# Performance work log

Measured on AMD Instinct MI355X. Metric: run time of the kernel, lower is better.

Reference implementation:

```python
import jax, jax.numpy as jnp
import numpy as np

N = 50000      # nodes
E = 1600000    # edges (avg degree 32)
IN, HID, OUT = 32, 32, 10
K = 2          # kernel_size (dim=1, degree=1 open B-spline -> basis (1-u, u))


def setup_inputs() -> dict:
    key = jax.random.key(0)
    ks = jax.random.split(key, 10)
    x = jax.random.normal(ks[0], (N, IN), dtype=jnp.float32)
    edge_index = jax.random.randint(ks[1], (2, E), 0, N, dtype=jnp.int64)
    edge_attr = jax.random.uniform(ks[2], (E, 1), dtype=jnp.float32)  # pseudo-coords in [0,1)
    s1 = 1.0 / np.sqrt(IN * K)
    s2 = 1.0 / np.sqrt(HID * K)
    W1 = jax.random.uniform(ks[3], (K, IN, HID), minval=-s1, maxval=s1, dtype=jnp.float32)
    root1 = jax.random.uniform(ks[4], (IN, HID), minval=-s1, maxval=s1, dtype=jnp.float32)
    b1 = jnp.zeros((HID,), jnp.float32)
    W2 = jax.random.uniform(ks[5], (K, HID, OUT), minval=-s2, maxval=s2, dtype=jnp.float32)
    root2 = jax.random.uniform(ks[6], (HID, OUT), minval=-s2, maxval=s2, dtype=jnp.float32)
    b2 = jnp.zeros((OUT,), jnp.float32)
    return {"x": x, "edge_index": edge_index, "edge_attr": edge_attr,
            "W1": W1, "root1": root1, "b1": b1,
            "W2": W2, "root2": root2, "b2": b2}


def spline_conv(x, edge_index, edge_attr, W, W_root, b):
    # SplineConv, dim=1, kernel_size=2, degree=1, aggr='mean', root_weight, bias.
    # Basis for pseudo u in [0,1): B_0(u) = 1-u, B_1(u) = u.
    src, dst = edge_index[0], edge_index[1]
    u = edge_attr[:, 0]                      # [E]
    h0 = x @ W[0]                            # [N, out] node-level transform, then gather
    h1 = x @ W[1]
    msg = (1.0 - u)[:, None] * h0[src] + u[:, None] * h1[src]   # [E, out]
    n = x.shape[0]
    agg = jax.ops.segment_sum(msg, dst, num_segments=n)
    deg = jax.ops.segment_sum(jnp.ones((src.shape[0],), x.dtype), dst, num_segments=n)
    mean = agg / jnp.maximum(deg, 1.0)[:, None]
    return mean + x @ W_root + b


def reference(x, edge_index, edge_attr, W1, root1, b1, W2, root2, b2):
    # Dropout is identity in eval mode.
    h = jax.nn.relu(spline_conv(x, edge_index, edge_attr, W1, root1, b1))
    h = spline_conv(h, edge_index, edge_attr, W2, root2, b2)
    return jax.nn.log_softmax(h, axis=1)
```

## Files before the change

kernel.cpp:

```cpp
#include <hip/hip_runtime.h>
#include <math.h>

#define GSHIFT 6
#define GSIZE  64
#define NBSZ   1024
#define EPB    4096
#define CAP    3072

#define UDEC1 0.00390625f
#define UDEC2 0.001953125f

__device__ __forceinline__ unsigned bf16rn(float f) {
    unsigned u = __float_as_uint(f);
    return (u + 0x7FFFu + ((u >> 16) & 1u)) >> 16;
}
__device__ __forceinline__ float bfl(unsigned v) { return __uint_as_float(v << 16); }
__device__ __forceinline__ float bfh(unsigned v) { return __uint_as_float(v & 0xFFFF0000u); }

__global__ __launch_bounds__(256) void k_prep(const float* __restrict__ x,
                                              unsigned* __restrict__ x_pk,
                                              int* __restrict__ bcount,
                                              int n, int NB) {
    int t = blockIdx.x * 256 + threadIdx.x;
    if (t < NB) bcount[t] = 0;
    if (t >= n) return;
    const float4* xp = (const float4*)(x + (size_t)t * 32);
    #pragma unroll
    for (int k = 0; k < 4; k++) {
        float4 a = xp[2 * k], c = xp[2 * k + 1];
        uint4 pk;
        pk.x = bf16rn(a.x) | (bf16rn(a.y) << 16);
        pk.y = bf16rn(a.z) | (bf16rn(a.w) << 16);
        pk.z = bf16rn(c.x) | (bf16rn(c.y) << 16);
        pk.w = bf16rn(c.z) | (bf16rn(c.w) << 16);
        *(uint4*)(x_pk + (size_t)t * 16 + k * 4) = pk;
    }
}

__global__ __launch_bounds__(1024) void k_part(const int* __restrict__ src,
                                               const int* __restrict__ dst,
                                               const float* __restrict__ attr,
                                               int* __restrict__ bcount,
                                               unsigned* __restrict__ su,
                                               int E_, int NB) {
    __shared__ int lh[NBSZ];
    __shared__ int lst[NBSZ];
    __shared__ int lcur[NBSZ];
    __shared__ int gbase[NBSZ];
    __shared__ int wsum[16];
    __shared__ __align__(16) unsigned srt[EPB];
    __shared__ unsigned short lbk[EPB];
    int tid = threadIdx.x, lane = tid & 63, w = tid >> 6;
    lh[tid] = 0;
    __syncthreads();
    int base = blockIdx.x * EPB;
    int d[4];
    unsigned rec[4];
    #pragma unroll
    for (int k = 0; k < 4; k++) {
        int e = base + k * 1024 + tid;
        bool val = e < E_;
        int dd = val ? dst[e] : 0;
        int s  = val ? src[e] : 0;
        float a = val ? attr[e] : 0.f;
        d[k] = val ? (dd >> GSHIFT) : -1;
        unsigned uq = (unsigned)(a * 256.0f);
        rec[k] = (unsigned)(s & 0xFFFF) | ((unsigned)(dd & (GSIZE - 1)) << 16) | (uq << 24);
        if (d[k] >= 0) atomicAdd(&lh[d[k]], 1);
    }
    __syncthreads();
    int v = lh[tid];
    int incl = v;
    #pragma unroll
    for (int o = 1; o < 64; o <<= 1) {
        int t2 = __shfl_up(incl, o);
        if (lane >= o) incl += t2;
    }
    if (lane == 63) wsum[w] = incl;
    __syncthreads();
    int woff = 0;
    for (int k = 0; k < w; k++) woff += wsum[k];
    int excl = woff + incl - v;
    lst[tid] = excl;
    lcur[tid] = excl;
    if (tid < NB) gbase[tid] = atomicAdd(&bcount[tid], v);
    __syncthreads();
    #pragma unroll
    for (int k = 0; k < 4; k++) {
        if (d[k] >= 0) {
            int pos = atomicAdd(&lcur[d[k]], 1);
            srt[pos] = rec[k];
            lbk[pos] = (unsigned short)d[k];
        }
    }
    __syncthreads();
    int total = E_ - base; if (total > EPB) total = EPB;
    for (int p = tid; p < total; p += 1024) {
        int b = lbk[p];
        su[(size_t)b * CAP + gbase[b] + (p - lst[b])] = srt[p];
    }
}

__global__ __launch_bounds__(512) void k_fused(const int* __restrict__ bcount,
                                               const unsigned* __restrict__ su,
                                               unsigned* __restrict__ su2,
                                               int* __restrict__ rowptr,
                                               int* __restrict__ deg,
                                               const unsigned* __restrict__ x_pk,
                                               const float* __restrict__ x,
                                               const float* __restrict__ W1,
                                               const float* __restrict__ root1,
                                               const float* __restrict__ b1,
                                               const float* __restrict__ W2,
                                               const float* __restrict__ root2,
                                               unsigned* __restrict__ gg,
                                               float* __restrict__ hr, int n) {
    __shared__ __align__(16) float sW0[1024], sDl[1024], sRt[1024];
    __shared__ float sA0[320], sD2[320], sR2[320], sB1[32];
    __shared__ __align__(16) unsigned sorted[CAP];
    __shared__ __align__(16) float accum[GSIZE * 64];
    __shared__ __align__(16) float xl[GSIZE * 32];
    __shared__ __align__(16) float hl[GSIZE * 32];
    __shared__ int hist[GSIZE], cur[GSIZE], sstart[GSIZE], sdeg[GSIZE];
    __shared__ int stot;

    int b = blockIdx.x, tid = threadIdx.x;
    size_t basee = (size_t)b * CAP;
    int cnt = bcount[b];
    int node0 = b << GSHIFT;

    if (tid < GSIZE) hist[tid] = 0;
    for (int i = tid; i < 1024; i += 512) {
        float w0 = W1[i];
        sW0[i] = w0; sDl[i] = W1[1024 + i] - w0; sRt[i] = root1[i];
    }
    for (int i = tid; i < 320; i += 512) {
        float a0 = W2[i];
        sA0[i] = a0; sD2[i] = W2[320 + i] - a0; sR2[i] = root2[i];
    }
    if (tid < 32) sB1[tid] = b1[tid];
    {
        size_t xbase = (size_t)node0 * 32;
        size_t xlim = (size_t)n * 32;
        for (int i = tid; i < GSIZE * 32; i += 512)
            xl[i] = (xbase + i < xlim) ? x[xbase + i] : 0.f;
    }
    __syncthreads();

    for (int e = tid; e < cnt; e += 512)
        atomicAdd(&hist[(su[basee + e] >> 16) & 63], 1);
    __syncthreads();

    if (tid < 64) {
        int v = hist[tid];
        int pv = (v + 3) & ~3;
        int incl = pv;
        #pragma unroll
        for (int o = 1; o < 64; o <<= 1) {
            int t2 = __shfl_up(incl, o);
            if (tid >= o) incl += t2;
        }
        int excl = incl - pv;
        cur[tid] = excl; sstart[tid] = excl; sdeg[tid] = v;
        int node = node0 + tid;
        if (node < n) { rowptr[node] = (int)basee + excl; deg[node] = v; }
        if (tid == 63) stot = excl + pv;
        for (int p = excl + v; p < excl + pv; p++) sorted[p] = 0;
    }
    __syncthreads();

    for (int e = tid; e < cnt; e += 512) {
        unsigned r = su[basee + e];
        int pos = atomicAdd(&cur[(r >> 16) & 63], 1);
        sorted[pos] = r;
    }
    __syncthreads();

    {
        int tot4 = stot >> 2;
        uint4* dp = (uint4*)(su2 + basee);
        for (int p = tid; p < tot4; p += 512)
            dp[p] = *(const uint4*)(sorted + p * 4);
    }
    {
        int nl = tid >> 3, q = tid & 3, half = (tid >> 2) & 1;
        int st = sstart[nl], dgi = sdeg[nl];
        int endl = st + dgi;
        int q4 = (dgi + 3) >> 2;
        int hq = q4 >> 1, rem = q4 & 1;
        int myq = hq + (half < rem ? 1 : 0);
        int e0 = st + (half * hq + min(half, rem)) * 4;
        float a0[8] = {0,0,0,0,0,0,0,0}, a1[8] = {0,0,0,0,0,0,0,0};
        for (int i = 0; i < myq; i++) {
            int e = e0 + i * 4;
            uint4 rq = *(const uint4*)(sorted + e);
            unsigned rr[4] = {rq.x, rq.y, rq.z, rq.w};
            #pragma unroll
            for (int k = 0; k < 4; k++) {
                bool v = (e + k) < endl;
                unsigned r = rr[k];
                uint4 g = *(const uint4*)(x_pk + (size_t)(r & 0xFFFFu) * 16 + q * 4);
                float wv = v ? 1.f : 0.f;
                float u = v ? fmaf((float)(r >> 24), UDEC1, UDEC2) : 0.f;
                unsigned gw[4] = {g.x, g.y, g.z, g.w};
                #pragma unroll
                for (int m2 = 0; m2 < 4; m2++) {
                    float fl = bfl(gw[m2]), fh = bfh(gw[m2]);
                    a0[2*m2]   = fmaf(wv, fl, a0[2*m2]);
                    a0[2*m2+1] = fmaf(wv, fh, a0[2*m2+1]);
                    a1[2*m2]   = fmaf(u, fl, a1[2*m2]);
                    a1[2*m2+1] = fmaf(u, fh, a1[2*m2+1]);
                }
            }
        }
        #pragma unroll
        for (int k = 0; k < 8; k++) {
            a0[k] += __shfl_xor(a0[k], 4);
            a1[k] += __shfl_xor(a1[k], 4);
        }
        if (half == 0) {
            #pragma unroll
            for (int k = 0; k < 8; k++) {
                accum[nl * 64 + q * 8 + k]      = a0[k];
                accum[nl * 64 + 32 + q * 8 + k] = a1[k];
            }
        }
    }
    __syncthreads();

    {
        int nl = tid >> 3, j = tid & 7;
        float invd = 1.0f / fmaxf((float)sdeg[nl], 1.0f);
        float4 hv = *(const float4*)(sB1 + 0);
        hv.x = sB1[4*j]; hv.y = sB1[4*j+1]; hv.z = sB1[4*j+2]; hv.w = sB1[4*j+3];
        for (int i = 0; i < 32; i++) {
            float s0 = accum[nl * 64 + i] * invd;
            float s1 = accum[nl * 64 + 32 + i] * invd;
            float xi = xl[nl * 32 + i];
            float4 w0 = *(const float4*)(sW0 + i * 32 + 4 * j);
            float4 dl = *(const float4*)(sDl + i * 32 + 4 * j);
            float4 rt = *(const float4*)(sRt + i * 32 + 4 * j);
            hv.x = fmaf(s0, w0.x, fmaf(s1, dl.x, fmaf(xi, rt.x, hv.x)));
            hv.y = fmaf(s0, w0.y, fmaf(s1, dl.y, fmaf(xi, rt.y, hv.y)));
            hv.z = fmaf(s0, w0.z, fmaf(s1, dl.z, fmaf(xi, rt.z, hv.z)));
            hv.w = fmaf(s0, w0.w, fmaf(s1, dl.w, fmaf(xi, rt.w, hv.w)));
        }
        hv.x = fmaxf(hv.x, 0.f); hv.y = fmaxf(hv.y, 0.f);
        hv.z = fmaxf(hv.z, 0.f); hv.w = fmaxf(hv.w, 0.f);
        *(float4*)(hl + nl * 32 + 4 * j) = hv;
    }
    __syncthreads();

    {
        int nl = tid >> 3, j = tid & 7;
        int node = node0 + nl;
        if (node < n) {
            #pragma unroll
            for (int ci = 0; ci < 2; ci++) {
                int c = j + ci * 8;
                if (c < 10) {
                    float g0 = 0.f, gd = 0.f, gr = 0.f;
                    for (int i = 0; i < 32; i++) {
                        float hi = hl[nl * 32 + i];
                        g0 = fmaf(hi, sA0[i * 10 + c], g0);
                        gd = fmaf(hi, sD2[i * 10 + c], gd);
                        gr = fmaf(hi, sR2[i * 10 + c], gr);
                    }
                    gg[(size_t)node * 16 + c] = bf16rn(g0) | (bf16rn(gd) << 16);
                    hr[(size_t)node * 10 + c] = gr;
                } else {
                    gg[(size_t)node * 16 + c] = 0;
                }
            }
        }
    }
}

__global__ __launch_bounds__(256) void k_agg2(const int* __restrict__ rowptr,
                                              const int* __restrict__ deg,
                                              const unsigned* __restrict__ su2,
                                              const unsigned* __restrict__ gg,
                                              const float* __restrict__ hr,
                                              const float* __restrict__ b2,
                                              float* __restrict__ out, int n) {
    int lane = threadIdx.x & 63;
    int node = (blockIdx.x * 4 + (threadIdx.x >> 6)) * 4 + (lane >> 4);
    int qt = (lane >> 2) & 3;
    int q  = lane & 3;
    if (node >= n) return;
    int start = rowptr[node], dgi = deg[node], end = start + dgi;
    int q4 = (dgi + 3) >> 2;
    int qb = q4 >> 2, rem = q4 & 3;
    int myq = qb + (qt < rem ? 1 : 0);
    int e0 = start + (qt * qb + min(qt, rem)) * 4;
    float acc[4] = {0, 0, 0, 0};
    for (int i = 0; i < myq; i++) {
        int e = e0 + i * 4;
        uint4 rq = *(const uint4*)(su2 + e);
        unsigned rr[4] = {rq.x, rq.y, rq.z, rq.w};
        #pragma unroll
        for (int k = 0; k < 4; k++) {
            bool v = (e + k) < end;
            unsigned r = rr[k];
            uint4 g = *(const uint4*)(gg + (size_t)(r & 0xFFFFu) * 16 + q * 4);
            float wv = v ? 1.f : 0.f;
            float u = v ? fmaf((float)(r >> 24), UDEC1, UDEC2) : 0.f;
            acc[0] = fmaf(wv, bfl(g.x), fmaf(u, bfh(g.x), acc[0]));
            acc[1] = fmaf(wv, bfl(g.y), fmaf(u, bfh(g.y), acc[1]));
            acc[2] = fmaf(wv, bfl(g.z), fmaf(u, bfh(g.z), acc[2]));
            acc[3] = fmaf(wv, bfl(g.w), fmaf(u, bfh(g.w), acc[3]));
        }
    }
    #pragma unroll
    for (int k = 0; k < 4; k++) {
        acc[k] += __shfl_xor(acc[k], 4);
        acc[k] += __shfl_xor(acc[k], 8);
    }
    float invd = 1.0f / fmaxf((float)dgi, 1.0f);
    int c0 = q * 4;
    float lg[4];
    float m = -INFINITY;
    #pragma unroll
    for (int k = 0; k < 4; k++) {
        int c = c0 + k;
        if (c < 10) {
            lg[k] = fmaf(acc[k], invd, hr[(size_t)node * 10 + c] + b2[c]);
            m = fmaxf(m, lg[k]);
        } else lg[k] = -INFINITY;
    }
    m = fmaxf(m, __shfl_xor(m, 1));
    m = fmaxf(m, __shfl_xor(m, 2));
    float ex = 0.f;
    #pragma unroll
    for (int k = 0; k < 4; k++)
        if (c0 + k < 10) ex += __expf(lg[k] - m);
    ex += __shfl_xor(ex, 1);
    ex += __shfl_xor(ex, 2);
    float lse = m + __logf(ex);
    if (qt == 0 && c0 < 10) {
        *(float2*)(out + (size_t)node * 10 + c0) =
            make_float2(lg[0] - lse, lg[1] - lse);
        if (c0 + 2 < 10)
            *(float2*)(out + (size_t)node * 10 + c0 + 2) =
                make_float2(lg[2] - lse, lg[3] - lse);
    }
}

extern "C" void kernel_launch(void* const* d_in, const int* in_sizes, int n_in,
                              void* d_out, int out_size, void* d_ws, size_t ws_size,
                              hipStream_t stream) {
    const float* x     = (const float*)d_in[0];
    const int*   ei    = (const int*)d_in[1];
    const float* attr  = (const float*)d_in[2];
    const float* W1    = (const float*)d_in[3];
    const float* root1 = (const float*)d_in[4];
    const float* b1    = (const float*)d_in[5];
    const float* W2    = (const float*)d_in[6];
    const float* root2 = (const float*)d_in[7];
    const float* b2    = (const float*)d_in[8];
    float* out = (float*)d_out;

    int N_ = in_sizes[0] / 32;
    int E_ = in_sizes[1] / 2;
    const int* src = ei;
    const int* dst = ei + E_;
    int NB = (N_ + GSIZE - 1) >> GSHIFT;
    int NP = (E_ + EPB - 1) / EPB;

    char* ws = (char*)d_ws;
    size_t off = 0;
    auto alloc = [&](size_t bytes) -> void* {
        void* p = ws + off;
        off += (bytes + 255) & ~(size_t)255;
        return p;
    };
    int*      bcount = (int*)     alloc((size_t)NB * 4);
    unsigned* su     = (unsigned*)alloc(((size_t)NB * CAP + 64) * 4);
    unsigned* su2    = (unsigned*)alloc(((size_t)NB * CAP + 64) * 4);
    int*      rowptr = (int*)     alloc((size_t)N_ * 4);
    int*      deg    = (int*)     alloc((size_t)N_ * 4);
    unsigned* x_pk   = (unsigned*)alloc((size_t)N_ * 16 * 4);
    unsigned* gg     = (unsigned*)alloc((size_t)N_ * 16 * 4);
    float*    hr     = (float*)   alloc((size_t)N_ * 10 * 4);

    int prep_blocks = (N_ > NB ? N_ : NB);
    k_prep <<<(prep_blocks + 255) / 256, 256, 0, stream>>>(x, x_pk, bcount, N_, NB);
    k_part <<<NP, 1024, 0, stream>>>(src, dst, attr, bcount, su, E_, NB);
    k_fused<<<NB, 512, 0, stream>>>(bcount, su, su2, rowptr, deg, x_pk, x,
                                    W1, root1, b1, W2, root2, gg, hr, N_);
    k_agg2 <<<(N_ + 15) / 16, 256, 0, stream>>>(rowptr, deg, su2, gg, hr, b2, out, N_);
}
```

Baseline: 82.33 us.

## Double k_fused block size to 1024 threads with 16 threads per node

The fused layer-1 kernel now launches 1024 threads per block instead of 512. In the gather, each node's edge quads are split over four thread groups instead of two, with an extra xor-shuffle reduction. The dense layer-1 and layer-2 transforms are remapped to 16 threads per node. This adds memory-level parallelism to the latency-bound gather and removes the two-pass loop in the layer-2 output. The cost is fewer resident blocks per CU, plus extra shuffles and per-thread work that becomes too small.

New measurement: 87.53 us. +6.3%, slower.

```diff
diff --git a/kernel.cpp b/kernel.cpp
--- a/kernel.cpp
+++ b/kernel.cpp
@@ -101,20 +101,20 @@
     }
 }
 
-__global__ __launch_bounds__(512) void k_fused(const int* __restrict__ bcount,
-                                               const unsigned* __restrict__ su,
-                                               unsigned* __restrict__ su2,
-                                               int* __restrict__ rowptr,
-                                               int* __restrict__ deg,
-                                               const unsigned* __restrict__ x_pk,
-                                               const float* __restrict__ x,
-                                               const float* __restrict__ W1,
-                                               const float* __restrict__ root1,
-                                               const float* __restrict__ b1,
-                                               const float* __restrict__ W2,
-                                               const float* __restrict__ root2,
-                                               unsigned* __restrict__ gg,
-                                               float* __restrict__ hr, int n) {
+__global__ __launch_bounds__(1024) void k_fused(const int* __restrict__ bcount,
+                                                const unsigned* __restrict__ su,
+                                                unsigned* __restrict__ su2,
+                                                int* __restrict__ rowptr,
+                                                int* __restrict__ deg,
+                                                const unsigned* __restrict__ x_pk,
+                                                const float* __restrict__ x,
+                                                const float* __restrict__ W1,
+                                                const float* __restrict__ root1,
+                                                const float* __restrict__ b1,
+                                                const float* __restrict__ W2,
+                                                const float* __restrict__ root2,
+                                                unsigned* __restrict__ gg,
+                                                float* __restrict__ hr, int n) {
     __shared__ __align__(16) float sW0[1024], sDl[1024], sRt[1024];
     __shared__ float sA0[320], sD2[320], sR2[320], sB1[32];
     __shared__ __align__(16) unsigned sorted[CAP];
@@ -130,24 +130,24 @@
     int node0 = b << GSHIFT;
 
     if (tid < GSIZE) hist[tid] = 0;
-    for (int i = tid; i < 1024; i += 512) {
-        float w0 = W1[i];
-        sW0[i] = w0; sDl[i] = W1[1024 + i] - w0; sRt[i] = root1[i];
-    }
-    for (int i = tid; i < 320; i += 512) {
-        float a0 = W2[i];
-        sA0[i] = a0; sD2[i] = W2[320 + i] - a0; sR2[i] = root2[i];
+    if (tid < 1024) {
+        float w0 = W1[tid];
+        sW0[tid] = w0; sDl[tid] = W1[1024 + tid] - w0; sRt[tid] = root1[tid];
+    }
+    if (tid < 320) {
+        float a0 = W2[tid];
+        sA0[tid] = a0; sD2[tid] = W2[320 + tid] - a0; sR2[tid] = root2[tid];
     }
     if (tid < 32) sB1[tid] = b1[tid];
     {
         size_t xbase = (size_t)node0 * 32;
         size_t xlim = (size_t)n * 32;
-        for (int i = tid; i < GSIZE * 32; i += 512)
+        for (int i = tid; i < GSIZE * 32; i += 1024)
             xl[i] = (xbase + i < xlim) ? x[xbase + i] : 0.f;
     }
     __syncthreads();
 
-    for (int e = tid; e < cnt; e += 512)
+    for (int e = tid; e < cnt; e += 1024)
         atomicAdd(&hist[(su[basee + e] >> 16) & 63], 1);
     __syncthreads();
 
@@ -169,7 +169,7 @@
     }
     __syncthreads();
 
-    for (int e = tid; e < cnt; e += 512) {
+    for (int e = tid; e < cnt; e += 1024) {
         unsigned r = su[basee + e];
         int pos = atomicAdd(&cur[(r >> 16) & 63], 1);
         sorted[pos] = r;
@@ -179,17 +179,17 @@
     {
         int tot4 = stot >> 2;
         uint4* dp = (uint4*)(su2 + basee);
-        for (int p = tid; p < tot4; p += 512)
+        for (int p = tid; p < tot4; p += 1024)
             dp[p] = *(const uint4*)(sorted + p * 4);
     }
     {
-        int nl = tid >> 3, q = tid & 3, half = (tid >> 2) & 1;
+        int nl = tid >> 4, qt = (tid >> 2) & 3, q = tid & 3;
         int st = sstart[nl], dgi = sdeg[nl];
         int endl = st + dgi;
         int q4 = (dgi + 3) >> 2;
-        int hq = q4 >> 1, rem = q4 & 1;
-        int myq = hq + (half < rem ? 1 : 0);
-        int e0 = st + (half * hq + min(half, rem)) * 4;
+        int qb = q4 >> 2, rem = q4 & 3;
+        int myq = qb + (qt < rem ? 1 : 0);
+        int e0 = st + (qt * qb + min(qt, rem)) * 4;
         float a0[8] = {0,0,0,0,0,0,0,0}, a1[8] = {0,0,0,0,0,0,0,0};
         for (int i = 0; i < myq; i++) {
             int e = e0 + i * 4;
@@ -217,8 +217,10 @@
         for (int k = 0; k < 8; k++) {
             a0[k] += __shfl_xor(a0[k], 4);
             a1[k] += __shfl_xor(a1[k], 4);
-        }
-        if (half == 0) {
+            a0[k] += __shfl_xor(a0[k], 8);
+            a1[k] += __shfl_xor(a1[k], 8);
+        }
+        if (qt == 0) {
             #pragma unroll
             for (int k = 0; k < 8; k++) {
                 accum[nl * 64 + q * 8 + k]      = a0[k];
@@ -229,48 +231,40 @@
     __syncthreads();
 
     {
-        int nl = tid >> 3, j = tid & 7;
+        int nl = tid >> 4, j = tid & 15;
         float invd = 1.0f / fmaxf((float)sdeg[nl], 1.0f);
-        float4 hv = *(const float4*)(sB1 + 0);
-        hv.x = sB1[4*j]; hv.y = sB1[4*j+1]; hv.z = sB1[4*j+2]; hv.w = sB1[4*j+3];
+        float hx = sB1[2*j], hy = sB1[2*j+1];
         for (int i = 0; i < 32; i++) {
             float s0 = accum[nl * 64 + i] * invd;
             float s1 = accum[nl * 64 + 32 + i] * invd;
             float xi = xl[nl * 32 + i];
-            float4 w0 = *(const float4*)(sW0 + i * 32 + 4 * j);
-            float4 dl = *(const float4*)(sDl + i * 32 + 4 * j);
-            float4 rt = *(const float4*)(sRt + i * 32 + 4 * j);
-            hv.x = fmaf(s0, w0.x, fmaf(s1, dl.x, fmaf(xi, rt.x, hv.x)));
-            hv.y = fmaf(s0, w0.y, fmaf(s1, dl.y, fmaf(xi, rt.y, hv.y)));
-            hv.z = fmaf(s0, w0.z, fmaf(s1, dl.z, fmaf(xi, rt.z, hv.z)));
-            hv.w = fmaf(s0, w0.w, fmaf(s1, dl.w, fmaf(xi, rt.w, hv.w)));
-        }
-        hv.x = fmaxf(hv.x, 0.f); hv.y = fmaxf(hv.y, 0.f);
-        hv.z = fmaxf(hv.z, 0.f); hv.w = fmaxf(hv.w, 0.f);
-        *(float4*)(hl + nl * 32 + 4 * j) = hv;
-    }
-    __syncthreads();
-
-    {
-        int nl = tid >> 3, j = tid & 7;
+            float2 w0 = *(const float2*)(sW0 + i * 32 + 2 * j);
+            float2 dl = *(const float2*)(sDl + i * 32 + 2 * j);
+            float2 rt = *(const float2*)(sRt + i * 32 + 2 * j);
+            hx = fmaf(s0, w0.x, fmaf(s1, dl.x, fmaf(xi, rt.x, hx)));
+            hy = fmaf(s0, w0.y, fmaf(s1, dl.y, fmaf(xi, rt.y, hy)));
+        }
+        hx = fmaxf(hx, 0.f); hy = fmaxf(hy, 0.f);
+        *(float2*)(hl + nl * 32 + 2 * j) = make_float2(hx, hy);
+    }
+    __syncthreads();
+
+    {
+        int nl = tid >> 4, c = tid & 15;
         int node = node0 + nl;
         if (node < n) {
-            #pragma unroll
-            for (int ci = 0; ci < 2; ci++) {
-                int c = j + ci * 8;
-                if (c < 10) {
-                    float g0 = 0.f, gd = 0.f, gr = 0.f;
-                    for (int i = 0; i < 32; i++) {
-                        float hi = hl[nl * 32 + i];
-                        g0 = fmaf(hi, sA0[i * 10 + c], g0);
-                        gd = fmaf(hi, sD2[i * 10 + c], gd);
-                        gr = fmaf(hi, sR2[i * 10 + c], gr);
-                    }
-                    gg[(size_t)node * 16 + c] = bf16rn(g0) | (bf16rn(gd) << 16);
-                    hr[(size_t)node * 10 + c] = gr;
-                } else {
-                    gg[(size_t)node * 16 + c] = 0;
+            if (c < 10) {
+                float g0 = 0.f, gd = 0.f, gr = 0.f;
+                for (int i = 0; i < 32; i++) {
+                    float hi = hl[nl * 32 + i];
+                    g0 = fmaf(hi, sA0[i * 10 + c], g0);
+                    gd = fmaf(hi, sD2[i * 10 + c], gd);
+                    gr = fmaf(hi, sR2[i * 10 + c], gr);
                 }
+                gg[(size_t)node * 16 + c] = bf16rn(g0) | (bf16rn(gd) << 16);
+                hr[(size_t)node * 10 + c] = gr;
+            } else {
+                gg[(size_t)node * 16 + c] = 0;
             }
         }
     }
@@ -386,7 +380,7 @@
     int prep_blocks = (N_ > NB ? N_ : NB);
     k_prep <<<(prep_blocks + 255) / 256, 256, 0, stream>>>(x, x_pk, bcount, N_, NB);
     k_part <<<NP, 1024, 0, stream>>>(src, dst, attr, bcount, su, E_, NB);
-    k_fused<<<NB, 512, 0, stream>>>(bcount, su, su2, rowptr, deg, x_pk, x,
-                                    W1, root1, b1, W2, root2, gg, hr, N_);
+    k_fused<<<NB, 1024, 0, stream>>>(bcount, su, su2, rowptr, deg, x_pk, x,
+                                     W1, root1, b1, W2, root2, gg, hr, N_);
     k_agg2 <<<(N_ + 15) / 16, 256, 0, stream>>>(rowptr, deg, su2, gg, hr, b2, out, N_);
 }
```

## Drop shared-memory weight staging and pack layer-1 accumulators as bf16 pairs

Applied to the files above, without the earlier changes.

Removes the per-block staging of W1, root1, W2, root2, b1 and the x tile into shared memory, and reads them straight from global memory (mostly L1/L2-cached) in the node transform loops. The per-node accumulator buffer is halved by storing both basis sums as a packed bf16 pair. Together this cuts LDS use substantially, which allows more resident blocks per CU and removes the prologue load phase. The cost is extra global loads in the inner loops and reduced precision of the aggregated sums before the dense transform.

New measurement: 93.28 us. 13.3% more time.

```diff
diff --git a/kernel.cpp b/kernel.cpp
--- a/kernel.cpp
+++ b/kernel.cpp
@@ -115,11 +115,8 @@
                                                const float* __restrict__ root2,
                                                unsigned* __restrict__ gg,
                                                float* __restrict__ hr, int n) {
-    __shared__ __align__(16) float sW0[1024], sDl[1024], sRt[1024];
-    __shared__ float sA0[320], sD2[320], sR2[320], sB1[32];
     __shared__ __align__(16) unsigned sorted[CAP];
-    __shared__ __align__(16) float accum[GSIZE * 64];
-    __shared__ __align__(16) float xl[GSIZE * 32];
+    __shared__ __align__(16) unsigned accum[GSIZE * 32];
     __shared__ __align__(16) float hl[GSIZE * 32];
     __shared__ int hist[GSIZE], cur[GSIZE], sstart[GSIZE], sdeg[GSIZE];
     __shared__ int stot;
@@ -130,21 +127,6 @@
     int node0 = b << GSHIFT;
 
     if (tid < GSIZE) hist[tid] = 0;
-    for (int i = tid; i < 1024; i += 512) {
-        float w0 = W1[i];
-        sW0[i] = w0; sDl[i] = W1[1024 + i] - w0; sRt[i] = root1[i];
-    }
-    for (int i = tid; i < 320; i += 512) {
-        float a0 = W2[i];
-        sA0[i] = a0; sD2[i] = W2[320 + i] - a0; sR2[i] = root2[i];
-    }
-    if (tid < 32) sB1[tid] = b1[tid];
-    {
-        size_t xbase = (size_t)node0 * 32;
-        size_t xlim = (size_t)n * 32;
-        for (int i = tid; i < GSIZE * 32; i += 512)
-            xl[i] = (xbase + i < xlim) ? x[xbase + i] : 0.f;
-    }
     __syncthreads();
 
     for (int e = tid; e < cnt; e += 512)
@@ -220,30 +202,30 @@
         }
         if (half == 0) {
             #pragma unroll
-            for (int k = 0; k < 8; k++) {
-                accum[nl * 64 + q * 8 + k]      = a0[k];
-                accum[nl * 64 + 32 + q * 8 + k] = a1[k];
-            }
+            for (int k = 0; k < 8; k++)
+                accum[nl * 32 + q * 8 + k] = bf16rn(a0[k]) | (bf16rn(a1[k]) << 16);
         }
     }
     __syncthreads();
 
     {
         int nl = tid >> 3, j = tid & 7;
+        int node = node0 + nl;
         float invd = 1.0f / fmaxf((float)sdeg[nl], 1.0f);
-        float4 hv = *(const float4*)(sB1 + 0);
-        hv.x = sB1[4*j]; hv.y = sB1[4*j+1]; hv.z = sB1[4*j+2]; hv.w = sB1[4*j+3];
+        float4 hv = *(const float4*)(b1 + 4 * j);
+        const float* xrow = x + (size_t)(node < n ? node : 0) * 32;
         for (int i = 0; i < 32; i++) {
-            float s0 = accum[nl * 64 + i] * invd;
-            float s1 = accum[nl * 64 + 32 + i] * invd;
-            float xi = xl[nl * 32 + i];
-            float4 w0 = *(const float4*)(sW0 + i * 32 + 4 * j);
-            float4 dl = *(const float4*)(sDl + i * 32 + 4 * j);
-            float4 rt = *(const float4*)(sRt + i * 32 + 4 * j);
-            hv.x = fmaf(s0, w0.x, fmaf(s1, dl.x, fmaf(xi, rt.x, hv.x)));
-            hv.y = fmaf(s0, w0.y, fmaf(s1, dl.y, fmaf(xi, rt.y, hv.y)));
-            hv.z = fmaf(s0, w0.z, fmaf(s1, dl.z, fmaf(xi, rt.z, hv.z)));
-            hv.w = fmaf(s0, w0.w, fmaf(s1, dl.w, fmaf(xi, rt.w, hv.w)));
+            unsigned sp = accum[nl * 32 + i];
+            float s0 = bfl(sp) * invd;
+            float s1 = bfh(sp) * invd;
+            float xi = xrow[i];
+            float4 w0 = *(const float4*)(W1 + i * 32 + 4 * j);
+            float4 w1 = *(const float4*)(W1 + 1024 + i * 32 + 4 * j);
+            float4 rt = *(const float4*)(root1 + i * 32 + 4 * j);
+            hv.x = fmaf(s0, w0.x, fmaf(s1, w1.x - w0.x, fmaf(xi, rt.x, hv.x)));
+            hv.y = fmaf(s0, w0.y, fmaf(s1, w1.y - w0.y, fmaf(xi, rt.y, hv.y)));
+            hv.z = fmaf(s0, w0.z, fmaf(s1, w1.z - w0.z, fmaf(xi, rt.z, hv.z)));
+            hv.w = fmaf(s0, w0.w, fmaf(s1, w1.w - w0.w, fmaf(xi, rt.w, hv.w)));
         }
         hv.x = fmaxf(hv.x, 0.f); hv.y = fmaxf(hv.y, 0.f);
         hv.z = fmaxf(hv.z, 0.f); hv.w = fmaxf(hv.w, 0.f);
@@ -262,9 +244,10 @@
                     float g0 = 0.f, gd = 0.f, gr = 0.f;
                     for (int i = 0; i < 32; i++) {
                         float hi = hl[nl * 32 + i];
-                        g0 = fmaf(hi, sA0[i * 10 + c], g0);
-                        gd = fmaf(hi, sD2[i * 10 + c], gd);
-                        gr = fmaf(hi, sR2[i * 10 + c], gr);
+                        float wa = W2[i * 10 + c];
+                        g0 = fmaf(hi, wa, g0);
+                        gd = fmaf(hi, W2[320 + i * 10 + c] - wa, gd);
+                        gr = fmaf(hi, root2[i * 10 + c], gr);
                     }
                     gg[(size_t)node * 16 + c] = bf16rn(g0) | (bf16rn(gd) << 16);
                     hr[(size_t)node * 10 + c] = gr;
```
